# Performance work log

Hardware: AMD Instinct MI355X
Metric: run time of the kernel (lower is better)

Reference implementation:

```python
import jax, jax.numpy as jnp
import numpy as np

NODE_SIZE = 40000
REL_SIZE = 2000
TRIPLE_SIZE = 600000
DIM = 128
DEPTH = 2
EPS = 1e-12


def _xavier(key, shape):
    lim = np.sqrt(6.0 / (shape[-2] + shape[-1]))
    return jax.random.uniform(key, shape, minval=-lim, maxval=lim, dtype=jnp.float32)


def _l2norm(x):
    # matches torch F.normalize(p=2, eps=1e-12)
    return x / jnp.maximum(jnp.linalg.norm(x, axis=-1, keepdims=True), EPS)


def _sparse_softmax(row, vals, n_rows):
    # torch.sparse.softmax over nonzeros of each row
    m = jax.ops.segment_max(vals, row, num_segments=n_rows)
    e = jnp.exp(vals - m[row])
    s = jax.ops.segment_sum(e, row, num_segments=n_rows)
    return e / s[row]


def _avg(adj, emb, n_rows):
    # sparse_coo(ones) -> sparse softmax over rows -> sparse mm  (== mean over neighbors)
    row, col = adj[0], adj[1]
    w = _sparse_softmax(row, jnp.zeros(row.shape, emb.dtype), n_rows)  # softmax of equal values
    return jax.ops.segment_sum(w[:, None] * emb[col], row, num_segments=n_rows)


def _nr_encoder(features, rel_emb, adj, r_index, r_val, triple_size, rel_size, node_size,
                attn, gate, proxy, bias):
    # NR_GraphAttention (Dual-AMN style relational reflection attention)
    row, col = adj[0], adj[1]
    # per-triple relation embedding: sparse [T, R] @ rel_emb
    tri_rel = jax.ops.segment_sum(r_val[:, None] * rel_emb[r_index[1]], r_index[0],
                                  num_segments=triple_size)
    tri_rel = _l2norm(tri_rel)  # [T, DIM]
    feats = jnp.tanh(features)
    outs = [feats]
    for l in range(DEPTH):
        neighs = feats[col]                                            # gather [T, DIM]
        neighs = neighs - 2.0 * jnp.sum(neighs * tri_rel, axis=-1, keepdims=True) * tri_rel
        att = _sparse_softmax(row, tri_rel @ attn[l][:, 0], node_size)  # edge attention
        feats = jnp.tanh(jax.ops.segment_sum(neighs * att[:, None], row,
                                             num_segments=node_size))  # scatter-sum
        outs.append(feats)
    out = jnp.concatenate(outs, axis=-1)                               # [N, DIM*(DEPTH+1)]
    # proxy matching + gating
    pa = jax.nn.softmax(_l2norm(out) @ _l2norm(proxy).T, axis=-1)
    pf = out - pa @ proxy
    g = jax.nn.sigmoid(pf @ gate + bias)
    return g * out + (1.0 - g) * pf


def setup_inputs() -> dict:
    ks = jax.random.split(jax.random.key(0), 16)
    ent_adj = jax.random.randint(ks[0], (2, TRIPLE_SIZE), 0, NODE_SIZE, dtype=jnp.int32)
    rel_adj = jnp.stack([jax.random.randint(ks[1], (TRIPLE_SIZE,), 0, NODE_SIZE, dtype=jnp.int32),
                         jax.random.randint(ks[2], (TRIPLE_SIZE,), 0, REL_SIZE, dtype=jnp.int32)])
    adj_list = jax.random.randint(ks[3], (2, TRIPLE_SIZE), 0, NODE_SIZE, dtype=jnp.int32)
    r_index = jnp.stack([jnp.arange(TRIPLE_SIZE, dtype=jnp.int32),
                         jax.random.randint(ks[4], (TRIPLE_SIZE,), 0, REL_SIZE, dtype=jnp.int32)])
    r_val = jax.random.uniform(ks[5], (TRIPLE_SIZE,), dtype=jnp.float32)
    mask = jnp.ones((NODE_SIZE,), dtype=jnp.int32)
    F3 = DIM * (DEPTH + 1)
    return dict(
        ent_adj=ent_adj, rel_adj=rel_adj, node_size=NODE_SIZE, rel_size=REL_SIZE,
        adj_list=adj_list, r_index=r_index, r_val=r_val, triple_size=TRIPLE_SIZE, mask=mask,
        ent_emb=_xavier(ks[6], (NODE_SIZE, DIM)),
        rel_emb=_xavier(ks[7], (REL_SIZE, DIM)),
        e_attn=_xavier(ks[8], (DEPTH, DIM, 1)), e_gate=_xavier(ks[9], (F3, F3)),
        e_proxy=_xavier(ks[10], (64, F3)), e_bias=jnp.zeros((1, F3), jnp.float32),
        r_attn=_xavier(ks[11], (DEPTH, DIM, 1)), r_gate=_xavier(ks[12], (F3, F3)),
        r_proxy=_xavier(ks[13], (64, F3)), r_bias=jnp.zeros((1, F3), jnp.float32),
    )


def reference(ent_adj, rel_adj, node_size, rel_size, adj_list, r_index, r_val, triple_size, mask,
              ent_emb, rel_emb, e_attn, e_gate, e_proxy, e_bias,
              r_attn, r_gate, r_proxy, r_bias):
    ent_feature = _avg(ent_adj, ent_emb, node_size)   # [N, DIM]
    rel_feature = _avg(rel_adj, rel_emb, node_size)   # [N, DIM]
    ent_feat = _nr_encoder(ent_feature, rel_emb, adj_list, r_index, r_val,
                           triple_size, rel_size, node_size, e_attn, e_gate, e_proxy, e_bias)
    rel_feat = _nr_encoder(rel_feature, rel_emb, adj_list, r_index, r_val,
                           triple_size, rel_size, node_size, r_attn, r_gate, r_proxy, r_bias)
    # dropout_rate = 0.0 -> identity
    return jnp.concatenate([ent_feat, rel_feat], axis=-1)  # [N, 768]
```

## Files before the change

### kernel.cpp

```cpp
#include <hip/hip_runtime.h>
#include <cmath>

#define NNODE 40000
#define NREL  2000
#define NTRI  600000
#define DIMK  128
#define F3    384
#define NPROX 64
#define EPSN  1e-12f
#define NSLICE 8
#define SLICE_ROWS (NNODE / NSLICE)

typedef unsigned short ushort_t;
typedef __attribute__((ext_vector_type(8))) short bf16x8;
typedef __attribute__((ext_vector_type(4))) float f32x4;

static __device__ __forceinline__ float waveSum(float v) {
#pragma unroll
    for (int m = 32; m >= 1; m >>= 1) v += __shfl_xor(v, m, 64);
    return v;
}

static __device__ __forceinline__ float bf2f(ushort_t h) {
    return __uint_as_float(((unsigned int)h) << 16);
}

static __device__ __forceinline__ void qreduce4(float4& v) {
#pragma unroll
    for (int m = 16; m <= 32; m <<= 1) {
        v.x += __shfl_xor(v.x, m, 64);
        v.y += __shfl_xor(v.y, m, 64);
        v.z += __shfl_xor(v.z, m, 64);
        v.w += __shfl_xor(v.w, m, 64);
    }
}

__global__ void k_count3(const int* __restrict__ rA, const int* __restrict__ rE,
                         const int* __restrict__ rR, int* __restrict__ dA,
                         int* __restrict__ dE, int* __restrict__ dR) {
    int t = blockIdx.x * 256 + threadIdx.x;
    if (t < NTRI) {
        atomicAdd(&dA[rA[t]], 1);
        atomicAdd(&dE[rE[t]], 1);
        atomicAdd(&dR[rR[t]], 1);
    }
}

__global__ void k_scan_fast(const int* __restrict__ dA, int* __restrict__ oA,
                            const int* __restrict__ dE, int* __restrict__ oE,
                            const int* __restrict__ dR, int* __restrict__ oR) {
    const int* deg = blockIdx.x == 0 ? dA : (blockIdx.x == 1 ? dE : dR);
    int* off = blockIdx.x == 0 ? oA : (blockIdx.x == 1 ? oE : oR);
    __shared__ int wsum[16];
    __shared__ int wpre[16];
    int tid = threadIdx.x;
    int lane = tid & 63, wv = tid >> 6;
    const int CH = 40;
    int base = tid * CH;
    int s = 0;
    for (int i = 0; i < CH; i++) {
        int idx = base + i;
        s += (idx < NNODE) ? deg[idx] : 0;
    }
    int incl = s;
#pragma unroll
    for (int m = 1; m < 64; m <<= 1) {
        int v = __shfl_up(incl, m, 64);
        if (lane >= m) incl += v;
    }
    if (lane == 63) wsum[wv] = incl;
    __syncthreads();
    if (tid < 16) {
        int v = wsum[tid];
#pragma unroll
        for (int m = 1; m < 16; m <<= 1) {
            int u = __shfl_up(v, m, 64);
            if (tid >= m) v += u;
        }
        wpre[tid] = v;
    }
    __syncthreads();
    int waveoff = (wv == 0) ? 0 : wpre[wv - 1];
    int run = waveoff + incl - s;
    for (int i = 0; i < CH; i++) {
        int idx = base + i;
        if (idx < NNODE) {
            off[idx] = run;
            run += deg[idx];
        }
    }
    if (tid == 0) off[NNODE] = wpre[15];
}

__global__ __launch_bounds__(256) void k_place_sliced(
    const int* __restrict__ rA, const int* __restrict__ cA,
    const int* __restrict__ rE, const int* __restrict__ cE,
    const int* __restrict__ rR, const int* __restrict__ cR,
    const int* __restrict__ ridx, const float* __restrict__ rval,
    const float* __restrict__ nrm,
    const int* __restrict__ oA, const int* __restrict__ oE, const int* __restrict__ oR,
    int* __restrict__ cntA, int* __restrict__ cntE, int* __restrict__ cntR,
    int2* __restrict__ ePackSc, int* __restrict__ eColE, int* __restrict__ eColR) {
    int slice = blockIdx.x & (NSLICE - 1);
    int t = (blockIdx.x >> 3) * 256 + threadIdx.x;
    if (t >= NTRI) return;
    int lo = slice * SLICE_ROWS;
    int r = rA[t];
    if ((unsigned)(r - lo) < (unsigned)SLICE_ROWS) {
        int rid = ridx[t];
        float v = rval[t];
        float sc = v / fmaxf(fabsf(v) * nrm[rid], EPSN);
        int p = oA[r] + atomicAdd(&cntA[r], 1);
        ePackSc[p] = make_int2(cA[t] | (rid << 16), __float_as_int(sc));
    }
    r = rE[t];
    if ((unsigned)(r - lo) < (unsigned)SLICE_ROWS)
        eColE[oE[r] + atomicAdd(&cntE[r], 1)] = cE[t];
    r = rR[t];
    if ((unsigned)(r - lo) < (unsigned)SLICE_ROWS)
        eColR[oR[r] + atomicAdd(&cntR[r], 1)] = cR[t];
}

__global__ void k_relprep(const float* __restrict__ rel_emb,
                          const float* __restrict__ e_attn, const float* __restrict__ r_attn,
                          float* __restrict__ nrm, float2* __restrict__ attL0,
                          float2* __restrict__ attL1) {
    int r = blockIdx.x;
    int lane = threadIdx.x;
    float a = rel_emb[r * DIMK + lane];
    float b = rel_emb[r * DIMK + 64 + lane];
    float nn = waveSum(a * a + b * b);
    float d0 = waveSum(a * e_attn[lane] + b * e_attn[64 + lane]);
    float d1 = waveSum(a * e_attn[DIMK + lane] + b * e_attn[DIMK + 64 + lane]);
    float d2 = waveSum(a * r_attn[lane] + b * r_attn[64 + lane]);
    float d3 = waveSum(a * r_attn[DIMK + lane] + b * r_attn[DIMK + 64 + lane]);
    if (lane == 0) {
        nrm[r] = sqrtf(nn);
        attL0[r] = make_float2(d0, d2);
        attL1[r] = make_float2(d1, d3);
    }
}

__global__ void k_proxyprep2(const float* __restrict__ e_proxy, const float* __restrict__ r_proxy,
                             float* __restrict__ pnT_e, float* __restrict__ pnT_r) {
    int enc = blockIdx.x >= NPROX;
    int k = blockIdx.x & (NPROX - 1);
    const float* proxy = enc ? r_proxy : e_proxy;
    float* pnT = enc ? pnT_r : pnT_e;
    int lane = threadIdx.x;
    float v[6];
    float ss = 0.f;
#pragma unroll
    for (int j = 0; j < 6; j++) {
        v[j] = proxy[k * F3 + j * 64 + lane];
        ss += v[j] * v[j];
    }
    ss = waveSum(ss);
    float inv = 1.0f / fmaxf(sqrtf(ss), EPSN);
#pragma unroll
    for (int j = 0; j < 6; j++) pnT[(j * 64 + lane) * NPROX + k] = v[j] * inv;
}

__global__ void k_gateprep2(const float* __restrict__ e_gate, const float* __restrict__ r_gate,
                            ushort_t* __restrict__ the, ushort_t* __restrict__ tle,
                            ushort_t* __restrict__ thr, ushort_t* __restrict__ tlr) {
    int enc = blockIdx.x >= F3;
    int k = enc ? blockIdx.x - F3 : blockIdx.x;
    const float* g = enc ? r_gate : e_gate;
    ushort_t* th = enc ? thr : the;
    ushort_t* tl = enc ? tlr : tle;
    int c = threadIdx.x;
    float v = g[(size_t)k * F3 + c];
    unsigned int b = __float_as_uint(v);
    th[(size_t)c * F3 + k] = (ushort_t)(b >> 16);
    float lo = v - __uint_as_float(b & 0xffff0000u);
    tl[(size_t)c * F3 + k] = (ushort_t)(__float_as_uint(lo) >> 16);
}

__global__ __launch_bounds__(256) void k_avg2(
    const int* __restrict__ offE, const int* __restrict__ eColE, const float* __restrict__ ent_emb,
    const int* __restrict__ offR, const int* __restrict__ eColR, const float* __restrict__ rel_emb,
    float* __restrict__ out_e, float* __restrict__ out_r) {
    int gw = (blockIdx.x * blockDim.x + threadIdx.x) >> 6;
    int lane = threadIdx.x & 63;
    if (gw >= 2 * NNODE) return;
    bool isR = gw >= NNODE;
    int wid = isR ? gw - NNODE : gw;
    const int* off = isR ? offR : offE;
    const int* ecol = isR ? eColR : eColE;
    const float4* emb4 = (const float4*)(isR ? rel_emb : ent_emb);
    float* outp = isR ? out_r : out_e;
    int q = lane >> 4, ql = lane & 15;
    int e0 = off[wid], e1 = off[wid + 1];
    float4 aA = {0, 0, 0, 0}, aB = {0, 0, 0, 0};
    for (int base = e0; base < e1; base += 64) {
        int n = min(64, e1 - base);
        int mc = (lane < n) ? ecol[base + lane] : -1;
        for (int j = 0; j < n; j += 4) {
            int e = j + q;
            int c = __shfl(mc, e, 64);
            if (e < n) {
                float4 va = emb4[(size_t)c * 32 + ql];
                float4 vb = emb4[(size_t)c * 32 + 16 + ql];
                aA.x += va.x; aA.y += va.y; aA.z += va.z; aA.w += va.w;
                aB.x += vb.x; aB.y += vb.y; aB.z += vb.z; aB.w += vb.w;
            }
        }
    }
    qreduce4(aA);
    qreduce4(aB);
    if (q == 0) {
        float invd = (e1 > e0) ? 1.0f / (float)(e1 - e0) : 0.0f;
        float4* o = (float4*)outp;
        float4 ra = {tanhf(aA.x * invd), tanhf(aA.y * invd), tanhf(aA.z * invd), tanhf(aA.w * invd)};
        float4 rb = {tanhf(aB.x * invd), tanhf(aB.y * invd), tanhf(aB.z * invd), tanhf(aB.w * invd)};
        o[(size_t)wid * 96 + ql] = ra;
        o[(size_t)wid * 96 + 16 + ql] = rb;
    }
}

__global__ __launch_bounds__(256) void k_agg2(
    const int* __restrict__ off, const int2* __restrict__ ePackSc,
    const float2* __restrict__ attL, const float* __restrict__ rel_emb,
    float* __restrict__ out_e, float* __restrict__ out_r, int lin) {
    int wid = (blockIdx.x * blockDim.x + threadIdx.x) >> 6;
    int lane = threadIdx.x & 63;
    if (wid >= NNODE) return;
    int q = lane >> 4, ql = lane & 15;
    int e0 = off[wid], e1 = off[wid + 1];
    const float4* rel4 = (const float4*)rel_emb;
    const float4* pe4 = (const float4*)out_e;
    const float4* pr4 = (const float4*)out_r;
    int sA = lin * 32 + ql, sB = lin * 32 + 16 + ql;
    float4 aEa = {0, 0, 0, 0}, aEb = {0, 0, 0, 0}, aRa = {0, 0, 0, 0}, aRb = {0, 0, 0, 0};
    float sE = 0.f, sR = 0.f;
    for (int base = e0; base < e1; base += 64) {
        int n = min(64, e1 - base);
        int pk = 0;
        float sc = 0.f, wE = 0.f, wR = 0.f;
        if (lane < n) {
            int2 ps = ePackSc[base + lane];
            pk = ps.x;
            sc = __int_as_float(ps.y);
            float2 a = attL[pk >> 16];
            wE = __expf(sc * a.x);
            wR = __expf(sc * a.y);
        }
        for (int j = 0; j < n; j += 4) {
            int e = j + q;
            int pke = __shfl(pk, e, 64);
            float sce = __shfl(sc, e, 64);
            float wEe = __shfl(wE, e, 64);
            float wRe = __shfl(wR, e, 64);
            int c = pke & 0xFFFF;
            int r = pke >> 16;
            float4 ra = rel4[(size_t)r * 32 + ql];
            float4 rb = rel4[(size_t)r * 32 + 16 + ql];
            float4 fa = pe4[(size_t)c * 96 + sA];
            float4 fb = pe4[(size_t)c * 96 + sB];
            float4 ga = pr4[(size_t)c * 96 + sA];
            float4 gb = pr4[(size_t)c * 96 + sB];
            float tax = sce * ra.x, tay = sce * ra.y, taz = sce * ra.z, taw = sce * ra.w;
            float tbx = sce * rb.x, tby = sce * rb.y, tbz = sce * rb.z, tbw = sce * rb.w;
            float dE = fa.x * tax + fa.y * tay + fa.z * taz + fa.w * taw +
                       fb.x * tbx + fb.y * tby + fb.z * tbz + fb.w * tbw;
            float dR = ga.x * tax + ga.y * tay + ga.z * taz + ga.w * taw +
                       gb.x * tbx + gb.y * tby + gb.z * tbz + gb.w * tbw;
#pragma unroll
            for (int m = 1; m <= 8; m <<= 1) {
                dE += __shfl_xor(dE, m, 64);
                dR += __shfl_xor(dR, m, 64);
            }
            dE *= 2.f;
            dR *= 2.f;
            aEa.x += wEe * (fa.x - dE * tax);
            aEa.y += wEe * (fa.y - dE * tay);
            aEa.z += wEe * (fa.z - dE * taz);
            aEa.w += wEe * (fa.w - dE * taw);
            aEb.x += wEe * (fb.x - dE * tbx);
            aEb.y += wEe * (fb.y - dE * tby);
            aEb.z += wEe * (fb.z - dE * tbz);
            aEb.w += wEe * (fb.w - dE * tbw);
            aRa.x += wRe * (ga.x - dR * tax);
            aRa.y += wRe * (ga.y - dR * tay);
            aRa.z += wRe * (ga.z - dR * taz);
            aRa.w += wRe * (ga.w - dR * taw);
            aRb.x += wRe * (gb.x - dR * tbx);
            aRb.y += wRe * (gb.y - dR * tby);
            aRb.z += wRe * (gb.z - dR * tbz);
            aRb.w += wRe * (gb.w - dR * tbw);
            sE += wEe;
            sR += wRe;
        }
    }
    qreduce4(aEa);
    qreduce4(aEb);
    qreduce4(aRa);
    qreduce4(aRb);
#pragma unroll
    for (int m = 16; m <= 32; m <<= 1) {
        sE += __shfl_xor(sE, m, 64);
        sR += __shfl_xor(sR, m, 64);
    }
    if (q == 0) {
        float iE = (e1 > e0) ? 1.f / sE : 0.f;
        float4* o = (float4*)out_e;
        float4 wa = {tanhf(aEa.x * iE), tanhf(aEa.y * iE), tanhf(aEa.z * iE), tanhf(aEa.w * iE)};
        float4 wb = {tanhf(aEb.x * iE), tanhf(aEb.y * iE), tanhf(aEb.z * iE), tanhf(aEb.w * iE)};
        o[(size_t)wid * 96 + (lin + 1) * 32 + ql] = wa;
        o[(size_t)wid * 96 + (lin + 1) * 32 + 16 + ql] = wb;
    } else if (q == 1) {
        float iR = (e1 > e0) ? 1.f / sR : 0.f;
        float4* o = (float4*)out_r;
        float4 wa = {tanhf(aRa.x * iR), tanhf(aRa.y * iR), tanhf(aRa.z * iR), tanhf(aRa.w * iR)};
        float4 wb = {tanhf(aRb.x * iR), tanhf(aRb.y * iR), tanhf(aRb.z * iR), tanhf(aRb.w * iR)};
        o[(size_t)wid * 96 + (lin + 1) * 32 + ql] = wa;
        o[(size_t)wid * 96 + (lin + 1) * 32 + 16 + ql] = wb;
    }
}

__global__ void k_scores(const float* __restrict__ out_e, const float* __restrict__ out_r,
                         const float* __restrict__ pnT_e, const float* __restrict__ pnT_r,
                         float* __restrict__ pa_e, float* __restrict__ pa_r) {
    const float* outb = blockIdx.z ? out_r : out_e;
    const float* pnT = blockIdx.z ? pnT_r : pnT_e;
    float* pa = blockIdx.z ? pa_r : pa_e;
    __shared__ __align__(16) float As[16][68];
    __shared__ __align__(16) float Bs[16][68];
    __shared__ float Ss[64][65];
    __shared__ float rnS[64];
    int tid = threadIdx.x;
    int row0 = blockIdx.x * 64;
    int kk = tid & 15, rr = tid >> 4;
    int cb = tid & 63, kb = tid >> 6;
    int tx = tid & 15, ty = tid >> 4;
    int c0 = tx * 4, r0 = ty * 4;
    float acc[4][4] = {};
    float ssp[4] = {};
    for (int k0 = 0; k0 < F3; k0 += 16) {
#pragma unroll
        for (int u = 0; u < 4; u++) {
            int r = rr + u * 16;
            float v = outb[(size_t)(row0 + r) * F3 + k0 + kk];
            As[kk][r] = v;
            ssp[u] += v * v;
        }
#pragma unroll
        for (int u = 0; u < 4; u++) {
            int k = kb + u * 4;
            Bs[k][cb] = pnT[(size_t)(k0 + k) * NPROX + cb];
        }
        __syncthreads();
#pragma unroll
        for (int k = 0; k < 16; k++) {
            float4 av = *(const float4*)&As[k][r0];
            float4 bv = *(const float4*)&Bs[k][c0];
            float a[4] = {av.x, av.y, av.z, av.w};
            float b[4] = {bv.x, bv.y, bv.z, bv.w};
#pragma unroll
            for (int i = 0; i < 4; i++)
#pragma unroll
                for (int j = 0; j < 4; j++) acc[i][j] += a[i] * b[j];
        }
        __syncthreads();
    }
#pragma unroll
    for (int u = 0; u < 4; u++) {
        float ss = ssp[u];
#pragma unroll
        for (int m = 1; m < 16; m <<= 1) ss += __shfl_xor(ss, m, 64);
        if (kk == 0) rnS[rr + u * 16] = 1.0f / fmaxf(sqrtf(ss), EPSN);
    }
    __syncthreads();
#pragma unroll
    for (int i = 0; i < 4; i++) {
        float rn = rnS[r0 + i];
#pragma unroll
        for (int j = 0; j < 4; j++) Ss[r0 + i][c0 + j] = acc[i][j] * rn;
    }
    __syncthreads();
    if (tid < 64) {
        int r = tid;
        float m = -1e30f;
        for (int c = 0; c < 64; c++) m = fmaxf(m, Ss[r][c]);
        float s = 0.f;
        for (int c = 0; c < 64; c++) s += expf(Ss[r][c] - m);
        float inv = 1.f / s;
        float* po = pa + (size_t)(row0 + r) * NPROX;
        for (int c = 0; c < 64; c++) po[c] = expf(Ss[r][c] - m) * inv;
    }
}

__global__ void k_pf(const float* __restrict__ pa_e, const float* __restrict__ pa_r,
                     const float* __restrict__ e_proxy, const float* __restrict__ r_proxy,
                     const float* __restrict__ out_e, const float* __restrict__ out_r,
                     ushort_t* __restrict__ pfh_e, ushort_t* __restrict__ pfl_e,
                     ushort_t* __restrict__ pfh_r, ushort_t* __restrict__ pfl_r) {
    const float* pa = blockIdx.z ? pa_r : pa_e;
    const float* proxy = blockIdx.z ? r_proxy : e_proxy;
    const float* outb = blockIdx.z ? out_r : out_e;
    ushort_t* pfh = blockIdx.z ? pfh_r : pfh_e;
    ushort_t* pfl = blockIdx.z ? pfl_r : pfl_e;
    __shared__ __align__(16) float As[16][68];
    __shared__ __align__(16) float Bs[16][68];
    int tid = threadIdx.x;
    int row0 = blockIdx.x * 64;
    int col0 = blockIdx.y * 64;
    int kk = tid & 15, rr = tid >> 4;
    int cb = tid & 63, kb = tid >> 6;
    int tx = tid & 15, ty = tid >> 4;
    int c0 = tx * 4, r0 = ty * 4;
    float acc[4][4] = {};
    for (int k0 = 0; k0 < NPROX; k0 += 16) {
#pragma unroll
        for (int u = 0; u < 4; u++) {
            int r = rr + u * 16;
            As[kk][r] = pa[(size_t)(row0 + r) * NPROX + k0 + kk];
        }
#pragma unroll
        for (int u = 0; u < 4; u++) {
            int k = kb + u * 4;
            Bs[k][cb] = proxy[(size_t)(k0 + k) * F3 + col0 + cb];
        }
        __syncthreads();
#pragma unroll
        for (int k = 0; k < 16; k++) {
            float4 av = *(const float4*)&As[k][r0];
            float4 bv = *(const float4*)&Bs[k][c0];
            float a[4] = {av.x, av.y, av.z, av.w};
            float b[4] = {bv.x, bv.y, bv.z, bv.w};
#pragma unroll
            for (int i = 0; i < 4; i++)
#pragma unroll
                for (int j = 0; j < 4; j++) acc[i][j] += a[i] * b[j];
        }
        __syncthreads();
    }
#pragma unroll
    for (int i = 0; i < 4; i++)
#pragma unroll
        for (int j = 0; j < 4; j++) {
            size_t idx = (size_t)(row0 + r0 + i) * F3 + col0 + c0 + j;
            float v = outb[idx] - acc[i][j];
            unsigned int b = __float_as_uint(v);
            pfh[idx] = (ushort_t)(b >> 16);
            float lo = v - __uint_as_float(b & 0xffff0000u);
            pfl[idx] = (ushort_t)(__float_as_uint(lo) >> 16);
        }
}

__global__ __launch_bounds__(256) void k_gate_mfma(
    const ushort_t* __restrict__ pfh_e, const ushort_t* __restrict__ pfl_e,
    const ushort_t* __restrict__ pfh_r, const ushort_t* __restrict__ pfl_r,
    const ushort_t* __restrict__ gTh_e, const ushort_t* __restrict__ gTl_e,
    const ushort_t* __restrict__ gTh_r, const ushort_t* __restrict__ gTl_r,
    const float* __restrict__ e_bias, const float* __restrict__ r_bias,
    const float* __restrict__ out_e, const float* __restrict__ out_r,
    float* __restrict__ dout) {
    const ushort_t* pfh = blockIdx.z ? pfh_r : pfh_e;
    const ushort_t* pfl = blockIdx.z ? pfl_r : pfl_e;
    const ushort_t* gTh = blockIdx.z ? gTh_r : gTh_e;
    const ushort_t* gTl = blockIdx.z ? gTl_r : gTl_e;
    const float* bias = blockIdx.z ? r_bias : e_bias;
    const float* outb = blockIdx.z ? out_r : out_e;
    int outoff = blockIdx.z ? F3 : 0;
    __shared__ __align__(16) ushort_t AsH[128 * 40];
    __shared__ __align__(16) ushort_t AsL[128 * 40];
    int tid = threadIdx.x;
    int w = tid >> 6, lane = tid & 63;
    int quad = lane >> 4, l16 = lane & 15;
    int wrow = (w >> 1) * 64, wcol = (w & 1) * 64;
    int gr0 = blockIdx.x * 128;
    int cb0 = blockIdx.y * 128;
    f32x4 acc[4][4];
#pragma unroll
    for (int rt = 0; rt < 4; rt++)
#pragma unroll
        for (int ct = 0; ct < 4; ct++) acc[rt][ct] = (f32x4){0.f, 0.f, 0.f, 0.f};

    int srow = tid >> 2, sseg = tid & 3;
    int gr_u0 = gr0 + srow;
    int gr_u1 = gr0 + srow + 64;
    uint4 pvh0, pvl0, pvh1, pvl1;
    {
        uint4 z = {0, 0, 0, 0};
        pvh0 = pvl0 = pvh1 = pvl1 = z;
        if (gr_u0 < NNODE) {
            pvh0 = *(const uint4*)&pfh[(size_t)gr_u0 * F3 + sseg * 8];
            pvl0 = *(const uint4*)&pfl[(size_t)gr_u0 * F3 + sseg * 8];
        }
        if (gr_u1 < NNODE) {
            pvh1 = *(const uint4*)&pfh[(size_t)gr_u1 * F3 + sseg * 8];
            pvl1 = *(const uint4*)&pfl[(size_t)gr_u1 * F3 + sseg * 8];
        }
    }
    for (int k0 = 0; k0 < F3; k0 += 32) {
        __syncthreads();
        *(uint4*)&AsH[srow * 40 + sseg * 8] = pvh0;
        *(uint4*)&AsL[srow * 40 + sseg * 8] = pvl0;
        *(uint4*)&AsH[(srow + 64) * 40 + sseg * 8] = pvh1;
        *(uint4*)&AsL[(srow + 64) * 40 + sseg * 8] = pvl1;
        bf16x8 bh[4], bl[4];
#pragma unroll
        for (int ct = 0; ct < 4; ct++) {
            int bc = cb0 + wcol + ct * 16 + l16;
            bh[ct] = *(const bf16x8*)&gTh[(size_t)bc * F3 + k0 + quad * 8];
            bl[ct] = *(const bf16x8*)&gTl[(size_t)bc * F3 + k0 + quad * 8];
        }
        int kn = k0 + 32;
        if (kn < F3) {
            if (gr_u0 < NNODE) {
                pvh0 = *(const uint4*)&pfh[(size_t)gr_u0 * F3 + kn + sseg * 8];
                pvl0 = *(const uint4*)&pfl[(size_t)gr_u0 * F3 + kn + sseg * 8];
            }
            if (gr_u1 < NNODE) {
                pvh1 = *(const uint4*)&pfh[(size_t)gr_u1 * F3 + kn + sseg * 8];
                pvl1 = *(const uint4*)&pfl[(size_t)gr_u1 * F3 + kn + sseg * 8];
            }
        }
        __syncthreads();
        bf16x8 ah[4], al[4];
#pragma unroll
        for (int rt = 0; rt < 4; rt++) {
            int ar = wrow + rt * 16 + l16;
            ah[rt] = *(const bf16x8*)&AsH[ar * 40 + quad * 8];
            al[rt] = *(const bf16x8*)&AsL[ar * 40 + quad * 8];
        }
#pragma unroll
        for (int rt = 0; rt < 4; rt++)
#pragma unroll
            for (int ct = 0; ct < 4; ct++) {
                acc[rt][ct] = __builtin_amdgcn_mfma_f32_16x16x32_bf16(ah[rt], bh[ct], acc[rt][ct], 0, 0, 0);
                acc[rt][ct] = __builtin_amdgcn_mfma_f32_16x16x32_bf16(ah[rt], bl[ct], acc[rt][ct], 0, 0, 0);
                acc[rt][ct] = __builtin_amdgcn_mfma_f32_16x16x32_bf16(al[rt], bh[ct], acc[rt][ct], 0, 0, 0);
            }
    }
#pragma unroll
    for (int rt = 0; rt < 4; rt++) {
        int rbase = gr0 + wrow + rt * 16 + quad * 4;
#pragma unroll
        for (int reg = 0; reg < 4; reg++) {
            int row = rbase + reg;
            if (row >= NNODE) continue;
#pragma unroll
            for (int ct = 0; ct < 4; ct++) {
                int c = cb0 + wcol + ct * 16 + l16;
                float x = acc[rt][ct][reg] + bias[c];
                float g = 1.f / (1.f + __expf(-x));
                size_t idx = (size_t)row * F3 + c;
                float pf = bf2f(pfh[idx]) + bf2f(pfl[idx]);
                float o = outb[idx];
                dout[(size_t)row * 768 + outoff + c] = g * o + (1.f - g) * pf;
            }
        }
    }
}

extern "C" void kernel_launch(void* const* d_in, const int* in_sizes, int n_in,
                              void* d_out, int out_size, void* d_ws, size_t ws_size,
                              hipStream_t stream) {
    const int* ent_adj = (const int*)d_in[0];
    const int* rel_adj = (const int*)d_in[1];
    const int* adj_list = (const int*)d_in[4];
    const int* r_index = (const int*)d_in[5];
    const float* r_val = (const float*)d_in[6];
    const float* ent_emb = (const float*)d_in[9];
    const float* rel_emb = (const float*)d_in[10];
    const float* e_attn = (const float*)d_in[11];
    const float* e_gate = (const float*)d_in[12];
    const float* e_proxy = (const float*)d_in[13];
    const float* e_bias = (const float*)d_in[14];
    const float* r_attn = (const float*)d_in[15];
    const float* r_gate = (const float*)d_in[16];
    const float* r_proxy = (const float*)d_in[17];
    const float* r_bias = (const float*)d_in[18];
    float* out = (float*)d_out;

    char* ws = (char*)d_ws;
    size_t off = 0;
    auto alloc = [&](size_t bytes) -> void* {
        off = (off + 255) & ~(size_t)255;
        void* p = ws + off;
        off += bytes;
        return p;
    };

    int* degcur = (int*)alloc(6 * NNODE * sizeof(int));
    int* degA = degcur, *curA = degcur + NNODE;
    int* degE = degcur + 2 * NNODE, *curE = degcur + 3 * NNODE;
    int* degR = degcur + 4 * NNODE, *curR = degcur + 5 * NNODE;
    int* offA = (int*)alloc((NNODE + 1) * sizeof(int));
    int* offE = (int*)alloc((NNODE + 1) * sizeof(int));
    int* offR = (int*)alloc((NNODE + 1) * sizeof(int));
    int2* ePackSc = (int2*)alloc(NTRI * sizeof(int2));
    int* eColE = (int*)alloc(NTRI * sizeof(int));
    int* eColR = (int*)alloc(NTRI * sizeof(int));
    float* nrm = (float*)alloc(NREL * sizeof(float));
    float2* attL0 = (float2*)alloc(NREL * sizeof(float2));
    float2* attL1 = (float2*)alloc(NREL * sizeof(float2));
    float* pnT_e = (float*)alloc((size_t)F3 * NPROX * sizeof(float));
    float* pnT_r = (float*)alloc((size_t)F3 * NPROX * sizeof(float));
    ushort_t* gTh_e = (ushort_t*)alloc((size_t)F3 * F3 * sizeof(ushort_t));
    ushort_t* gTl_e = (ushort_t*)alloc((size_t)F3 * F3 * sizeof(ushort_t));
    ushort_t* gTh_r = (ushort_t*)alloc((size_t)F3 * F3 * sizeof(ushort_t));
    ushort_t* gTl_r = (ushort_t*)alloc((size_t)F3 * F3 * sizeof(ushort_t));
    float* pa_e = (float*)alloc((size_t)NNODE * NPROX * sizeof(float));
    float* pa_r = (float*)alloc((size_t)NNODE * NPROX * sizeof(float));
    ushort_t* pfh_e = (ushort_t*)alloc((size_t)NNODE * F3 * sizeof(ushort_t));
    ushort_t* pfl_e = (ushort_t*)alloc((size_t)NNODE * F3 * sizeof(ushort_t));
    ushort_t* pfh_r = (ushort_t*)alloc((size_t)NNODE * F3 * sizeof(ushort_t));
    ushort_t* pfl_r = (ushort_t*)alloc((size_t)NNODE * F3 * sizeof(ushort_t));
    float* out_e = (float*)alloc((size_t)NNODE * F3 * sizeof(float));
    float* out_r = (float*)alloc((size_t)NNODE * F3 * sizeof(float));
    (void)ws_size; (void)in_sizes; (void)n_in; (void)out_size;

    hipMemsetAsync(degcur, 0, 6 * NNODE * sizeof(int), stream);

    int gT = (NTRI + 255) / 256;
    k_count3<<<gT, 256, 0, stream>>>(adj_list, ent_adj, rel_adj, degA, degE, degR);
    k_scan_fast<<<3, 1024, 0, stream>>>(degA, offA, degE, offE, degR, offR);
    k_relprep<<<NREL, 64, 0, stream>>>(rel_emb, e_attn, r_attn, nrm, attL0, attL1);
    k_place_sliced<<<gT * NSLICE, 256, 0, stream>>>(
        adj_list, adj_list + NTRI, ent_adj, ent_adj + NTRI, rel_adj, rel_adj + NTRI,
        r_index + NTRI, r_val, nrm, offA, offE, offR, curA, curE, curR,
        ePackSc, eColE, eColR);
    k_proxyprep2<<<2 * NPROX, 64, 0, stream>>>(e_proxy, r_proxy, pnT_e, pnT_r);
    k_gateprep2<<<2 * F3, F3, 0, stream>>>(e_gate, r_gate, gTh_e, gTl_e, gTh_r, gTl_r);

    k_avg2<<<(2 * NNODE) / 4, 256, 0, stream>>>(offE, eColE, ent_emb, offR, eColR, rel_emb,
                                                out_e, out_r);

    int gW = NNODE / 4;
    k_agg2<<<gW, 256, 0, stream>>>(offA, ePackSc, attL0, rel_emb, out_e, out_r, 0);
    k_agg2<<<gW, 256, 0, stream>>>(offA, ePackSc, attL1, rel_emb, out_e, out_r, 1);

    dim3 gS(NNODE / 64, 1, 2);
    dim3 gP(NNODE / 64, F3 / 64, 2);
    dim3 gG((NNODE + 127) / 128, F3 / 128, 2);
    k_scores<<<gS, 256, 0, stream>>>(out_e, out_r, pnT_e, pnT_r, pa_e, pa_r);
    k_pf<<<gP, 256, 0, stream>>>(pa_e, pa_r, e_proxy, r_proxy, out_e, out_r,
                                 pfh_e, pfl_e, pfh_r, pfl_r);
    k_gate_mfma<<<gG, 256, 0, stream>>>(pfh_e, pfl_e, pfh_r, pfl_r, gTh_e, gTl_e, gTh_r, gTl_r,
                                        e_bias, r_bias, out_e, out_r, out);
}
```

Before: 993.8 us.

## Fold proxy subtraction into gate GEMM via precomputed proxy@gate and drop k_pf

Rewrites pf@gate as out@gate - pa@(proxy@gate), precomputing proxy@gate and proxy in split-bf16 form. The k_pf kernel and the pf hi/lo intermediates are removed. The gate kernel now reads fp32 out directly, splits it to hi/lo bf16 on the fly, and adds two small K=64 MFMA passes for the gate correction and pa@proxy. The output becomes out - (1-g)*pa@proxy. This saves a full N×384 GEMM pass plus large intermediate writes and reads, in exchange for a narrower column tile (64) with more blocks and some in-loop conversion work.

```diff
diff --git a/kernel.cpp b/kernel.cpp
--- a/kernel.cpp
+++ b/kernel.cpp
@@ -21,10 +21,6 @@
     return v;
 }
 
-static __device__ __forceinline__ float bf2f(ushort_t h) {
-    return __uint_as_float(((unsigned int)h) << 16);
-}
-
 static __device__ __forceinline__ void qreduce4(float4& v) {
 #pragma unroll
     for (int m = 16; m <= 32; m <<= 1) {
@@ -33,6 +29,25 @@
         v.z += __shfl_xor(v.z, m, 64);
         v.w += __shfl_xor(v.w, m, 64);
     }
+}
+
+static __device__ __forceinline__ uint2 splitpair(float x, float y) {
+    unsigned int bx = __float_as_uint(x), by = __float_as_uint(y);
+    unsigned int h = (bx >> 16) | (by & 0xffff0000u);
+    float lx = x - __uint_as_float(bx & 0xffff0000u);
+    float ly = y - __uint_as_float(by & 0xffff0000u);
+    unsigned int l = (__float_as_uint(lx) >> 16) | (__float_as_uint(ly) & 0xffff0000u);
+    return make_uint2(h, l);
+}
+
+static __device__ __forceinline__ void pack8(const float4& a, const float4& b,
+                                             uint4& h, uint4& l) {
+    uint2 p0 = splitpair(a.x, a.y);
+    uint2 p1 = splitpair(a.z, a.w);
+    uint2 p2 = splitpair(b.x, b.y);
+    uint2 p3 = splitpair(b.z, b.w);
+    h = make_uint4(p0.x, p1.x, p2.x, p3.x);
+    l = make_uint4(p0.y, p1.y, p2.y, p3.y);
 }
 
 __global__ void k_count3(const int* __restrict__ rA, const int* __restrict__ rE,
@@ -175,6 +190,35 @@
     th[(size_t)c * F3 + k] = (ushort_t)(b >> 16);
     float lo = v - __uint_as_float(b & 0xffff0000u);
     tl[(size_t)c * F3 + k] = (ushort_t)(__float_as_uint(lo) >> 16);
+}
+
+__global__ void k_pgprep(const float* __restrict__ e_proxy, const float* __restrict__ r_proxy,
+                         const float* __restrict__ e_gate, const float* __restrict__ r_gate,
+                         ushort_t* __restrict__ pgTh_e, ushort_t* __restrict__ pgTl_e,
+                         ushort_t* __restrict__ prTh_e, ushort_t* __restrict__ prTl_e,
+                         ushort_t* __restrict__ pgTh_r, ushort_t* __restrict__ pgTl_r,
+                         ushort_t* __restrict__ prTh_r, ushort_t* __restrict__ prTl_r) {
+    int enc = blockIdx.y;
+    const float* proxy = enc ? r_proxy : e_proxy;
+    const float* gate = enc ? r_gate : e_gate;
+    ushort_t* pgTh = enc ? pgTh_r : pgTh_e;
+    ushort_t* pgTl = enc ? pgTl_r : pgTl_e;
+    ushort_t* prTh = enc ? prTh_r : prTh_e;
+    ushort_t* prTl = enc ? prTl_r : prTl_e;
+    int c = blockIdx.x;
+    int p = threadIdx.x;
+    float s = 0.f;
+    for (int k = 0; k < F3; k++) s = fmaf(proxy[p * F3 + k], gate[(size_t)k * F3 + c], s);
+    float v = -s;
+    unsigned int b = __float_as_uint(v);
+    pgTh[c * NPROX + p] = (ushort_t)(b >> 16);
+    float lo = v - __uint_as_float(b & 0xffff0000u);
+    pgTl[c * NPROX + p] = (ushort_t)(__float_as_uint(lo) >> 16);
+    float pv = proxy[p * F3 + c];
+    unsigned int pb = __float_as_uint(pv);
+    prTh[c * NPROX + p] = (ushort_t)(pb >> 16);
+    float plo = pv - __uint_as_float(pb & 0xffff0000u);
+    prTl[c * NPROX + p] = (ushort_t)(__float_as_uint(plo) >> 16);
 }
 
 __global__ __launch_bounds__(256) void k_avg2(
@@ -321,10 +365,12 @@
 
 __global__ void k_scores(const float* __restrict__ out_e, const float* __restrict__ out_r,
                          const float* __restrict__ pnT_e, const float* __restrict__ pnT_r,
-                         float* __restrict__ pa_e, float* __restrict__ pa_r) {
+                         ushort_t* __restrict__ paH_e, ushort_t* __restrict__ paL_e,
+                         ushort_t* __restrict__ paH_r, ushort_t* __restrict__ paL_r) {
     const float* outb = blockIdx.z ? out_r : out_e;
     const float* pnT = blockIdx.z ? pnT_r : pnT_e;
-    float* pa = blockIdx.z ? pa_r : pa_e;
+    ushort_t* paH = blockIdx.z ? paH_r : paH_e;
+    ushort_t* paL = blockIdx.z ? paL_r : paL_e;
     __shared__ __align__(16) float As[16][68];
     __shared__ __align__(16) float Bs[16][68];
     __shared__ float Ss[64][65];
@@ -386,81 +432,37 @@
         float s = 0.f;
         for (int c = 0; c < 64; c++) s += expf(Ss[r][c] - m);
         float inv = 1.f / s;
-        float* po = pa + (size_t)(row0 + r) * NPROX;
-        for (int c = 0; c < 64; c++) po[c] = expf(Ss[r][c] - m) * inv;
-    }
-}
-
-__global__ void k_pf(const float* __restrict__ pa_e, const float* __restrict__ pa_r,
-                     const float* __restrict__ e_proxy, const float* __restrict__ r_proxy,
-                     const float* __restrict__ out_e, const float* __restrict__ out_r,
-                     ushort_t* __restrict__ pfh_e, ushort_t* __restrict__ pfl_e,
-                     ushort_t* __restrict__ pfh_r, ushort_t* __restrict__ pfl_r) {
-    const float* pa = blockIdx.z ? pa_r : pa_e;
-    const float* proxy = blockIdx.z ? r_proxy : e_proxy;
-    const float* outb = blockIdx.z ? out_r : out_e;
-    ushort_t* pfh = blockIdx.z ? pfh_r : pfh_e;
-    ushort_t* pfl = blockIdx.z ? pfl_r : pfl_e;
-    __shared__ __align__(16) float As[16][68];
-    __shared__ __align__(16) float Bs[16][68];
-    int tid = threadIdx.x;
-    int row0 = blockIdx.x * 64;
-    int col0 = blockIdx.y * 64;
-    int kk = tid & 15, rr = tid >> 4;
-    int cb = tid & 63, kb = tid >> 6;
-    int tx = tid & 15, ty = tid >> 4;
-    int c0 = tx * 4, r0 = ty * 4;
-    float acc[4][4] = {};
-    for (int k0 = 0; k0 < NPROX; k0 += 16) {
-#pragma unroll
-        for (int u = 0; u < 4; u++) {
-            int r = rr + u * 16;
-            As[kk][r] = pa[(size_t)(row0 + r) * NPROX + k0 + kk];
-        }
-#pragma unroll
-        for (int u = 0; u < 4; u++) {
-            int k = kb + u * 4;
-            Bs[k][cb] = proxy[(size_t)(k0 + k) * F3 + col0 + cb];
-        }
-        __syncthreads();
-#pragma unroll
-        for (int k = 0; k < 16; k++) {
-            float4 av = *(const float4*)&As[k][r0];
-            float4 bv = *(const float4*)&Bs[k][c0];
-            float a[4] = {av.x, av.y, av.z, av.w};
-            float b[4] = {bv.x, bv.y, bv.z, bv.w};
-#pragma unroll
-            for (int i = 0; i < 4; i++)
-#pragma unroll
-                for (int j = 0; j < 4; j++) acc[i][j] += a[i] * b[j];
-        }
-        __syncthreads();
-    }
-#pragma unroll
-    for (int i = 0; i < 4; i++)
-#pragma unroll
-        for (int j = 0; j < 4; j++) {
-            size_t idx = (size_t)(row0 + r0 + i) * F3 + col0 + c0 + j;
-            float v = outb[idx] - acc[i][j];
+        size_t base = (size_t)(row0 + r) * NPROX;
+        for (int c = 0; c < 64; c++) {
+            float v = expf(Ss[r][c] - m) * inv;
             unsigned int b = __float_as_uint(v);
-            pfh[idx] = (ushort_t)(b >> 16);
+            paH[base + c] = (ushort_t)(b >> 16);
             float lo = v - __uint_as_float(b & 0xffff0000u);
-            pfl[idx] = (ushort_t)(__float_as_uint(lo) >> 16);
-        }
-}
-
-__global__ __launch_bounds__(256) void k_gate_mfma(
-    const ushort_t* __restrict__ pfh_e, const ushort_t* __restrict__ pfl_e,
-    const ushort_t* __restrict__ pfh_r, const ushort_t* __restrict__ pfl_r,
+            paL[base + c] = (ushort_t)(__float_as_uint(lo) >> 16);
+        }
+    }
+}
+
+__global__ __launch_bounds__(256) void k_gate_fused(
+    const ushort_t* __restrict__ paH_e, const ushort_t* __restrict__ paL_e,
+    const ushort_t* __restrict__ paH_r, const ushort_t* __restrict__ paL_r,
     const ushort_t* __restrict__ gTh_e, const ushort_t* __restrict__ gTl_e,
     const ushort_t* __restrict__ gTh_r, const ushort_t* __restrict__ gTl_r,
+    const ushort_t* __restrict__ pgTh_e, const ushort_t* __restrict__ pgTl_e,
+    const ushort_t* __restrict__ prTh_e, const ushort_t* __restrict__ prTl_e,
+    const ushort_t* __restrict__ pgTh_r, const ushort_t* __restrict__ pgTl_r,
+    const ushort_t* __restrict__ prTh_r, const ushort_t* __restrict__ prTl_r,
     const float* __restrict__ e_bias, const float* __restrict__ r_bias,
     const float* __restrict__ out_e, const float* __restrict__ out_r,
     float* __restrict__ dout) {
-    const ushort_t* pfh = blockIdx.z ? pfh_r : pfh_e;
-    const ushort_t* pfl = blockIdx.z ? pfl_r : pfl_e;
+    const ushort_t* paH = blockIdx.z ? paH_r : paH_e;
+    const ushort_t* paL = blockIdx.z ? paL_r : paL_e;
     const ushort_t* gTh = blockIdx.z ? gTh_r : gTh_e;
     const ushort_t* gTl = blockIdx.z ? gTl_r : gTl_e;
+    const ushort_t* pgTh = blockIdx.z ? pgTh_r : pgTh_e;
+    const ushort_t* pgTl = blockIdx.z ? pgTl_r : pgTl_e;
+    const ushort_t* prTh = blockIdx.z ? prTh_r : prTh_e;
+    const ushort_t* prTl = blockIdx.z ? prTl_r : prTl_e;
     const float* bias = blockIdx.z ? r_bias : e_bias;
     const float* outb = blockIdx.z ? out_r : out_e;
     int outoff = blockIdx.z ? F3 : 0;
@@ -469,40 +471,46 @@
     int tid = threadIdx.x;
     int w = tid >> 6, lane = tid & 63;
     int quad = lane >> 4, l16 = lane & 15;
-    int wrow = (w >> 1) * 64, wcol = (w & 1) * 64;
+    int wrow = (w >> 1) * 64, wcol = (w & 1) * 32;
     int gr0 = blockIdx.x * 128;
-    int cb0 = blockIdx.y * 128;
-    f32x4 acc[4][4];
+    int cb0 = blockIdx.y * 64;
+    f32x4 accg[4][2], accp[4][2];
 #pragma unroll
     for (int rt = 0; rt < 4; rt++)
 #pragma unroll
-        for (int ct = 0; ct < 4; ct++) acc[rt][ct] = (f32x4){0.f, 0.f, 0.f, 0.f};
+        for (int ct = 0; ct < 2; ct++) {
+            accg[rt][ct] = (f32x4){0.f, 0.f, 0.f, 0.f};
+            accp[rt][ct] = (f32x4){0.f, 0.f, 0.f, 0.f};
+        }
 
     int srow = tid >> 2, sseg = tid & 3;
     int gr_u0 = gr0 + srow;
     int gr_u1 = gr0 + srow + 64;
-    uint4 pvh0, pvl0, pvh1, pvl1;
+    float4 p0a, p0b, p1a, p1b;
     {
-        uint4 z = {0, 0, 0, 0};
-        pvh0 = pvl0 = pvh1 = pvl1 = z;
+        float4 z = {0, 0, 0, 0};
+        p0a = p0b = p1a = p1b = z;
         if (gr_u0 < NNODE) {
-            pvh0 = *(const uint4*)&pfh[(size_t)gr_u0 * F3 + sseg * 8];
-            pvl0 = *(const uint4*)&pfl[(size_t)gr_u0 * F3 + sseg * 8];
+            p0a = *(const float4*)&outb[(size_t)gr_u0 * F3 + sseg * 8];
+            p0b = *(const float4*)&outb[(size_t)gr_u0 * F3 + sseg * 8 + 4];
         }
         if (gr_u1 < NNODE) {
-            pvh1 = *(const uint4*)&pfh[(size_t)gr_u1 * F3 + sseg * 8];
-            pvl1 = *(const uint4*)&pfl[(size_t)gr_u1 * F3 + sseg * 8];
+            p1a = *(const float4*)&outb[(size_t)gr_u1 * F3 + sseg * 8];
+            p1b = *(const float4*)&outb[(size_t)gr_u1 * F3 + sseg * 8 + 4];
         }
     }
     for (int k0 = 0; k0 < F3; k0 += 32) {
         __syncthreads();
-        *(uint4*)&AsH[srow * 40 + sseg * 8] = pvh0;
-        *(uint4*)&AsL[srow * 40 + sseg * 8] = pvl0;
-        *(uint4*)&AsH[(srow + 64) * 40 + sseg * 8] = pvh1;
-        *(uint4*)&AsL[(srow + 64) * 40 + sseg * 8] = pvl1;
-        bf16x8 bh[4], bl[4];
-#pragma unroll
-        for (int ct = 0; ct < 4; ct++) {
+        uint4 h0, l0, h1, l1;
+        pack8(p0a, p0b, h0, l0);
+        pack8(p1a, p1b, h1, l1);
+        *(uint4*)&AsH[srow * 40 + sseg * 8] = h0;
+        *(uint4*)&AsL[srow * 40 + sseg * 8] = l0;
+        *(uint4*)&AsH[(srow + 64) * 40 + sseg * 8] = h1;
+        *(uint4*)&AsL[(srow + 64) * 40 + sseg * 8] = l1;
+        bf16x8 bh[2], bl[2];
+#pragma unroll
+        for (int ct = 0; ct < 2; ct++) {
             int bc = cb0 + wcol + ct * 16 + l16;
             bh[ct] = *(const bf16x8*)&gTh[(size_t)bc * F3 + k0 + quad * 8];
             bl[ct] = *(const bf16x8*)&gTl[(size_t)bc * F3 + k0 + quad * 8];
@@ -510,12 +518,12 @@
         int kn = k0 + 32;
         if (kn < F3) {
             if (gr_u0 < NNODE) {
-                pvh0 = *(const uint4*)&pfh[(size_t)gr_u0 * F3 + kn + sseg * 8];
-                pvl0 = *(const uint4*)&pfl[(size_t)gr_u0 * F3 + kn + sseg * 8];
+                p0a = *(const float4*)&outb[(size_t)gr_u0 * F3 + kn + sseg * 8];
+                p0b = *(const float4*)&outb[(size_t)gr_u0 * F3 + kn + sseg * 8 + 4];
             }
             if (gr_u1 < NNODE) {
-                pvh1 = *(const uint4*)&pfh[(size_t)gr_u1 * F3 + kn + sseg * 8];
-                pvl1 = *(const uint4*)&pfl[(size_t)gr_u1 * F3 + kn + sseg * 8];
+                p1a = *(const float4*)&outb[(size_t)gr_u1 * F3 + kn + sseg * 8];
+                p1b = *(const float4*)&outb[(size_t)gr_u1 * F3 + kn + sseg * 8 + 4];
             }
         }
         __syncthreads();
@@ -529,10 +537,47 @@
 #pragma unroll
         for (int rt = 0; rt < 4; rt++)
 #pragma unroll
-            for (int ct = 0; ct < 4; ct++) {
-                acc[rt][ct] = __builtin_amdgcn_mfma_f32_16x16x32_bf16(ah[rt], bh[ct], acc[rt][ct], 0, 0, 0);
-                acc[rt][ct] = __builtin_amdgcn_mfma_f32_16x16x32_bf16(ah[rt], bl[ct], acc[rt][ct], 0, 0, 0);
-                acc[rt][ct] = __builtin_amdgcn_mfma_f32_16x16x32_bf16(al[rt], bh[ct], acc[rt][ct], 0, 0, 0);
+            for (int ct = 0; ct < 2; ct++) {
+                accg[rt][ct] = __builtin_amdgcn_mfma_f32_16x16x32_bf16(ah[rt], bh[ct], accg[rt][ct], 0, 0, 0);
+                accg[rt][ct] = __builtin_amdgcn_mfma_f32_16x16x32_bf16(ah[rt], bl[ct], accg[rt][ct], 0, 0, 0);
+                accg[rt][ct] = __builtin_amdgcn_mfma_f32_16x16x32_bf16(al[rt], bh[ct], accg[rt][ct], 0, 0, 0);
+            }
+    }
+    const bf16x8 zz = (bf16x8){0, 0, 0, 0, 0, 0, 0, 0};
+#pragma unroll
+    for (int kp = 0; kp < 2; kp++) {
+        int kp0 = kp * 32;
+        bf16x8 pah[4], pal[4];
+#pragma unroll
+        for (int rt = 0; rt < 4; rt++) {
+            int ar = gr0 + wrow + rt * 16 + l16;
+            if (ar < NNODE) {
+                pah[rt] = *(const bf16x8*)&paH[(size_t)ar * NPROX + kp0 + quad * 8];
+                pal[rt] = *(const bf16x8*)&paL[(size_t)ar * NPROX + kp0 + quad * 8];
+            } else {
+                pah[rt] = zz;
+                pal[rt] = zz;
+            }
+        }
+        bf16x8 pgh[2], pgl[2], prh[2], prl[2];
+#pragma unroll
+        for (int ct = 0; ct < 2; ct++) {
+            int bc = cb0 + wcol + ct * 16 + l16;
+            pgh[ct] = *(const bf16x8*)&pgTh[(size_t)bc * NPROX + kp0 + quad * 8];
+            pgl[ct] = *(const bf16x8*)&pgTl[(size_t)bc * NPROX + kp0 + quad * 8];
+            prh[ct] = *(const bf16x8*)&prTh[(size_t)bc * NPROX + kp0 + quad * 8];
+            prl[ct] = *(const bf16x8*)&prTl[(size_t)bc * NPROX + kp0 + quad * 8];
+        }
+#pragma unroll
+        for (int rt = 0; rt < 4; rt++)
+#pragma unroll
+            for (int ct = 0; ct < 2; ct++) {
+                accg[rt][ct] = __builtin_amdgcn_mfma_f32_16x16x32_bf16(pah[rt], pgh[ct], accg[rt][ct], 0, 0, 0);
+                accg[rt][ct] = __builtin_amdgcn_mfma_f32_16x16x32_bf16(pah[rt], pgl[ct], accg[rt][ct], 0, 0, 0);
+                accg[rt][ct] = __builtin_amdgcn_mfma_f32_16x16x32_bf16(pal[rt], pgh[ct], accg[rt][ct], 0, 0, 0);
+                accp[rt][ct] = __builtin_amdgcn_mfma_f32_16x16x32_bf16(pah[rt], prh[ct], accp[rt][ct], 0, 0, 0);
+                accp[rt][ct] = __builtin_amdgcn_mfma_f32_16x16x32_bf16(pah[rt], prl[ct], accp[rt][ct], 0, 0, 0);
+                accp[rt][ct] = __builtin_amdgcn_mfma_f32_16x16x32_bf16(pal[rt], prh[ct], accp[rt][ct], 0, 0, 0);
             }
     }
 #pragma unroll
@@ -543,14 +588,13 @@
             int row = rbase + reg;
             if (row >= NNODE) continue;
 #pragma unroll
-            for (int ct = 0; ct < 4; ct++) {
+            for (int ct = 0; ct < 2; ct++) {
                 int c = cb0 + wcol + ct * 16 + l16;
-                float x = acc[rt][ct][reg] + bias[c];
+                float x = accg[rt][ct][reg] + bias[c];
                 float g = 1.f / (1.f + __expf(-x));
-                size_t idx = (size_t)row * F3 + c;
-                float pf = bf2f(pfh[idx]) + bf2f(pfl[idx]);
-                float o = outb[idx];
-                dout[(size_t)row * 768 + outoff + c] = g * o + (1.f - g) * pf;
+                float o = outb[(size_t)row * F3 + c];
+                float z = accp[rt][ct][reg];
+                dout[(size_t)row * 768 + outoff + c] = o - (1.f - g) * z;
             }
         }
     }
@@ -604,12 +648,18 @@
     ushort_t* gTl_e = (ushort_t*)alloc((size_t)F3 * F3 * sizeof(ushort_t));
     ushort_t* gTh_r = (ushort_t*)alloc((size_t)F3 * F3 * sizeof(ushort_t));
     ushort_t* gTl_r = (ushort_t*)alloc((size_t)F3 * F3 * sizeof(ushort_t));
-    float* pa_e = (float*)alloc((size_t)NNODE * NPROX * sizeof(float));
-    float* pa_r = (float*)alloc((size_t)NNODE * NPROX * sizeof(float));
-    ushort_t* pfh_e = (ushort_t*)alloc((size_t)NNODE * F3 * sizeof(ushort_t));
-    ushort_t* pfl_e = (ushort_t*)alloc((size_t)NNODE * F3 * sizeof(ushort_t));
-    ushort_t* pfh_r = (ushort_t*)alloc((size_t)NNODE * F3 * sizeof(ushort_t));
-    ushort_t* pfl_r = (ushort_t*)alloc((size_t)NNODE * F3 * sizeof(ushort_t));
+    ushort_t* pgTh_e = (ushort_t*)alloc((size_t)F3 * NPROX * sizeof(ushort_t));
+    ushort_t* pgTl_e = (ushort_t*)alloc((size_t)F3 * NPROX * sizeof(ushort_t));
+    ushort_t* prTh_e = (ushort_t*)alloc((size_t)F3 * NPROX * sizeof(ushort_t));
+    ushort_t* prTl_e = (ushort_t*)alloc((size_t)F3 * NPROX * sizeof(ushort_t));
+    ushort_t* pgTh_r = (ushort_t*)alloc((size_t)F3 * NPROX * sizeof(ushort_t));
+    ushort_t* pgTl_r = (ushort_t*)alloc((size_t)F3 * NPROX * sizeof(ushort_t));
+    ushort_t* prTh_r = (ushort_t*)alloc((size_t)F3 * NPROX * sizeof(ushort_t));
+    ushort_t* prTl_r = (ushort_t*)alloc((size_t)F3 * NPROX * sizeof(ushort_t));
+    ushort_t* paH_e = (ushort_t*)alloc((size_t)NNODE * NPROX * sizeof(ushort_t));
+    ushort_t* paL_e = (ushort_t*)alloc((size_t)NNODE * NPROX * sizeof(ushort_t));
+    ushort_t* paH_r = (ushort_t*)alloc((size_t)NNODE * NPROX * sizeof(ushort_t));
+    ushort_t* paL_r = (ushort_t*)alloc((size_t)NNODE * NPROX * sizeof(ushort_t));
     float* out_e = (float*)alloc((size_t)NNODE * F3 * sizeof(float));
     float* out_r = (float*)alloc((size_t)NNODE * F3 * sizeof(float));
     (void)ws_size; (void)in_sizes; (void)n_in; (void)out_size;
@@ -626,6 +676,9 @@
         ePackSc, eColE, eColR);
     k_proxyprep2<<<2 * NPROX, 64, 0, stream>>>(e_proxy, r_proxy, pnT_e, pnT_r);
     k_gateprep2<<<2 * F3, F3, 0, stream>>>(e_gate, r_gate, gTh_e, gTl_e, gTh_r, gTl_r);
+    k_pgprep<<<dim3(F3, 2), 64, 0, stream>>>(e_proxy, r_proxy, e_gate, r_gate,
+                                             pgTh_e, pgTl_e, prTh_e, prTl_e,
+                                             pgTh_r, pgTl_r, prTh_r, prTl_r);
 
     k_avg2<<<(2 * NNODE) / 4, 256, 0, stream>>>(offE, eColE, ent_emb, offR, eColR, rel_emb,
                                                 out_e, out_r);
@@ -635,11 +688,12 @@
     k_agg2<<<gW, 256, 0, stream>>>(offA, ePackSc, attL1, rel_emb, out_e, out_r, 1);
 
     dim3 gS(NNODE / 64, 1, 2);
-    dim3 gP(NNODE / 64, F3 / 64, 2);
-    dim3 gG((NNODE + 127) / 128, F3 / 128, 2);
-    k_scores<<<gS, 256, 0, stream>>>(out_e, out_r, pnT_e, pnT_r, pa_e, pa_r);
-    k_pf<<<gP, 256, 0, stream>>>(pa_e, pa_r, e_proxy, r_proxy, out_e, out_r,
-                                 pfh_e, pfl_e, pfh_r, pfl_r);
-    k_gate_mfma<<<gG, 256, 0, stream>>>(pfh_e, pfl_e, pfh_r, pfl_r, gTh_e, gTl_e, gTh_r, gTl_r,
-                                        e_bias, r_bias, out_e, out_r, out);
-}
+    dim3 gG((NNODE + 127) / 128, F3 / 64, 2);
+    k_scores<<<gS, 256, 0, stream>>>(out_e, out_r, pnT_e, pnT_r,
+                                     paH_e, paL_e, paH_r, paL_r);
+    k_gate_fused<<<gG, 256, 0, stream>>>(paH_e, paL_e, paH_r, paL_r,
+                                         gTh_e, gTl_e, gTh_r, gTl_r,
+                                         pgTh_e, pgTl_e, prTh_e, prTl_e,
+                                         pgTh_r, pgTl_r, prTh_r, prTl_r,
+                                         e_bias, r_bias, out_e, out_r, out);
+}
```

Result: faster. 949.1 us (-4.5%).
